# Kernel tuning notes

Measured on AMD Instinct MI355X. Metric: run time of the kernel, lower is better.

Reference implementation:

```python
import jax, jax.numpy as jnp
import numpy as np

N_NODES = 100000
N_EDGES = 1600000
D_IN = 128
D_HID = 128
D_OUT = 40


def _linear_init(key, fan_in, fan_out):
    # torch nn.Linear default: U(-1/sqrt(fan_in), 1/sqrt(fan_in)) for W and b
    kw, kb = jax.random.split(key)
    bound = 1.0 / np.sqrt(fan_in)
    W = jax.random.uniform(kw, (fan_in, fan_out), jnp.float32, -bound, bound)
    b = jax.random.uniform(kb, (fan_out,), jnp.float32, -bound, bound)
    return W, b


def setup_inputs() -> dict:
    key = jax.random.key(0)
    ks = jax.random.split(key, 8)
    x = jax.random.normal(ks[0], (N_NODES, D_IN), jnp.float32)
    edges = jax.random.randint(ks[1], (2, N_EDGES), 0, N_NODES, jnp.int64)
    # layer 0: MLP(128 -> 128 -> 128)
    W1_0, b1_0 = _linear_init(ks[2], D_IN, D_HID)
    W2_0, b2_0 = _linear_init(ks[3], D_HID, D_HID)
    # layer 1: MLP(128 -> 128 -> 128)
    W1_1, b1_1 = _linear_init(ks[4], D_HID, D_HID)
    W2_1, b2_1 = _linear_init(ks[5], D_HID, D_HID)
    # layer 2: MLP(128 -> 128 -> 40)
    W1_2, b1_2 = _linear_init(ks[6], D_HID, D_HID)
    W2_2, b2_2 = _linear_init(ks[7], D_HID, D_OUT)
    eps = jnp.zeros(())  # GINConv train_eps=True initializes eps=0
    return {
        "x": x, "edges": edges,
        "W1_0": W1_0, "b1_0": b1_0, "W2_0": W2_0, "b2_0": b2_0, "eps_0": eps,
        "W1_1": W1_1, "b1_1": b1_1, "W2_1": W2_1, "b2_1": b2_1, "eps_1": eps,
        "W1_2": W1_2, "b1_2": b1_2, "W2_2": W2_2, "b2_2": b2_2, "eps_2": eps,
    }


def _gin_conv(x, src, dst, eps, W1, b1, W2, b2):
    # sum-aggregate neighbor features: out_i = MLP((1+eps)*x_i + sum_{j->i} x_j)
    aggr = jax.ops.segment_sum(x[src], dst, num_segments=x.shape[0])
    h = (1.0 + eps) * x + aggr
    h = jnp.maximum(h @ W1 + b1, 0.0)  # MLP layer 1 + ReLU
    return h @ W2 + b2                  # MLP layer 2


def reference(x, edges,
              W1_0, b1_0, W2_0, b2_0, eps_0,
              W1_1, b1_1, W2_1, b2_1, eps_1,
              W1_2, b1_2, W2_2, b2_2, eps_2):
    src, dst = edges[0], edges[1]
    # dropout is identity at inference (training=False)
    h = jax.nn.relu(_gin_conv(x, src, dst, eps_0, W1_0, b1_0, W2_0, b2_0))
    h = jax.nn.relu(_gin_conv(h, src, dst, eps_1, W1_1, b1_1, W2_1, b2_1))
    o = _gin_conv(h, src, dst, eps_2, W1_2, b1_2, W2_2, b2_2)
    return jax.nn.log_softmax(o, axis=1)
```

## Files before the change

kernel.cpp:

```cpp
#include <hip/hip_runtime.h>
#include <stdint.h>

typedef __attribute__((ext_vector_type(8))) short short8;
typedef __attribute__((ext_vector_type(4))) short short4v;
typedef __attribute__((ext_vector_type(4))) float float4v;

__device__ __forceinline__ float bf2f(unsigned short s) {
    union { unsigned int u; float f; } c; c.u = ((unsigned int)s) << 16; return c.f;
}
__device__ __forceinline__ unsigned short f2bf(float f) {
    union { float f; unsigned int u; } c; c.f = f;
    unsigned int x = c.u;
    unsigned int r = x + 0x7fffu + ((x >> 16) & 1u);
    return (unsigned short)(r >> 16);
}
__device__ __forceinline__ void unpack2(unsigned int u, float& lo, float& hi) {
    union { unsigned int uu; float ff; } a, b;
    a.uu = u << 16;
    b.uu = u & 0xffff0000u;
    lo = a.ff; hi = b.ff;
}


__global__ __launch_bounds__(512) void bs_scan(const int* __restrict__ bucketCnt,
                                               int* __restrict__ bucketBase,
                                               int* __restrict__ bucketCur,
                                               int* __restrict__ off, int M, int nE) {
    __shared__ int s[512];
    int t = threadIdx.x;
    int v = bucketCnt[t];
    s[t] = v;
    __syncthreads();
    for (int o = 1; o < 512; o <<= 1) {
        int x = (t >= o) ? s[t - o] : 0;
        __syncthreads();
        s[t] += x;
        __syncthreads();
    }
    bucketBase[t] = s[t] - v;
    bucketCur[t] = s[t] - v;
    if (t == 511) bucketBase[512] = s[511];
    if (t == 0) off[M] = nE;
}

__global__ __launch_bounds__(512) void bs_scatter(const int* __restrict__ src,
                                                  const int* __restrict__ dst, int nE,
                                                  int* __restrict__ bucketCur,
                                                  unsigned int* __restrict__ ebuf) {
    __shared__ int cnt[512];
    __shared__ int excl[512];
    __shared__ int chunk[512];
    __shared__ unsigned int buf[4096];
    __shared__ unsigned short bkt[4096];
    int t = threadIdx.x;
    cnt[t] = 0;
    __syncthreads();
    int base = blockIdx.x * 4096;
    int n = nE - base; if (n > 4096) n = 4096;
    unsigned int pk[8]; int bk[8]; int rk[8];
#pragma unroll
    for (int u = 0; u < 8; ++u) {
        int i = t + u * 512;
        if (i < n) {
            int e = base + i;
            int d = dst[e];
            int b = d >> 8;
            bk[u] = b;
            pk[u] = (unsigned int)src[e] | ((unsigned int)(d & 255) << 17);
            rk[u] = atomicAdd(&cnt[b], 1);
        } else bk[u] = -1;
    }
    __syncthreads();
    excl[t] = cnt[t];
    __syncthreads();
    for (int o = 1; o < 512; o <<= 1) {
        int x = (t >= o) ? excl[t - o] : 0;
        __syncthreads();
        excl[t] += x;
        __syncthreads();
    }
    int ex = excl[t] - cnt[t];
    __syncthreads();
    excl[t] = ex;
    if (cnt[t]) chunk[t] = atomicAdd(&bucketCur[t], cnt[t]);
    __syncthreads();
#pragma unroll
    for (int u = 0; u < 8; ++u) {
        if (bk[u] >= 0) {
            int lp = excl[bk[u]] + rk[u];
            buf[lp] = pk[u];
            bkt[lp] = (unsigned short)bk[u];
        }
    }
    __syncthreads();
    for (int i = t; i < n; i += 512) {
        int b = bkt[i];
        ebuf[chunk[b] + (i - excl[b])] = buf[i];
    }
}

__global__ __launch_bounds__(512) void bs_build(const unsigned int* __restrict__ ebuf,
                                                const int* __restrict__ bucketBase,
                                                int* __restrict__ off,
                                                int* __restrict__ esrc, int M) {
    __shared__ int cnt[256];
    __shared__ int excl[256];
    __shared__ int obuf[5120];
    int t = threadIdx.x, b = blockIdx.x;
    int base = bucketBase[b];
    int n = bucketBase[b + 1] - base;
    if (t < 256) cnt[t] = 0;
    __syncthreads();
    unsigned int pk[10]; int dl[10]; int rk[10];
#pragma unroll
    for (int u = 0; u < 10; ++u) {
        int i = t + u * 512;
        if (i < n) {
            unsigned int p = ebuf[base + i];
            pk[u] = p;
            int d = (p >> 17) & 255;
            dl[u] = d;
            rk[u] = atomicAdd(&cnt[d], 1);
        } else dl[u] = -1;
    }
    __syncthreads();
    if (t < 256) excl[t] = cnt[t];
    __syncthreads();
    for (int o = 1; o < 256; o <<= 1) {
        int x = (t < 256 && t >= o) ? excl[t - o] : 0;
        __syncthreads();
        if (t < 256) excl[t] += x;
        __syncthreads();
    }
    if (t < 256) {
        int ex = excl[t] - cnt[t];
        int node = b * 256 + t;
        if (node < M) off[node] = base + ex;
        excl[t] = ex;
    }
    __syncthreads();
#pragma unroll
    for (int u = 0; u < 10; ++u) {
        if (dl[u] >= 0) {
            int lp = excl[dl[u]] + rk[u];
            if (lp < 5120) obuf[lp] = (int)(pk[u] & 0x1FFFF);
        }
    }
    __syncthreads();
    for (int i = t; i < n; i += 512) esrc[base + i] = obuf[i];
}

struct Prep {
    const float* W[6];
    unsigned short* hi[6];
    const float4* xin;
    uint2* xout;
    int n4;
    int nxBlocks;
    const int* dst;
    int nE;
    int* bucketCnt;
};

__global__ __launch_bounds__(256) void k_prep(Prep p) {
    __shared__ int c[512];
    int b = blockIdx.x;
    int t = threadIdx.x;
    if (b < 344) {
        int mat = b >> 6;
        int rel = b - mat * 64;
        int NPAD = (mat == 5) ? 48 : 128;
        int N = (mat == 5) ? 40 : 128;
        int idx = rel * 256 + t;
        if (idx >= NPAD * 128) return;
        int n = idx >> 7, k = idx & 127;
        float w = (n < N) ? p.W[mat][k * N + n] : 0.f;
        p.hi[mat][idx] = f2bf(w);
    } else if (b < 344 + p.nxBlocks) {
        int i = (b - 344) * 256 + t;
        if (i >= p.n4) return;
        float4 v = p.xin[i];
        uint2 o;
        o.x = ((unsigned int)f2bf(v.y) << 16) | f2bf(v.x);
        o.y = ((unsigned int)f2bf(v.w) << 16) | f2bf(v.z);
        p.xout[i] = o;
    } else {
        for (int i = t; i < 512; i += 256) c[i] = 0;
        __syncthreads();
        int base = (b - 344 - p.nxBlocks) * 4096;
        for (int i = t; i < 4096; i += 256) {
            int e = base + i;
            if (e < p.nE) atomicAdd(&c[p.dst[e] >> 8], 1);
        }
        __syncthreads();
        for (int i = t; i < 512; i += 256)
            if (c[i]) atomicAdd(&p.bucketCnt[i], c[i]);
    }
}

__device__ __forceinline__ void acc8(uint4 v, float* s) {
    float a, b;
    unpack2(v.x, a, b); s[0] += a; s[1] += b;
    unpack2(v.y, a, b); s[2] += a; s[3] += b;
    unpack2(v.z, a, b); s[4] += a; s[5] += b;
    unpack2(v.w, a, b); s[6] += a; s[7] += b;
}

__global__ __launch_bounds__(256) void k_aggr(const uint4* __restrict__ Hin,
                                              const int* __restrict__ off,
                                              const int* __restrict__ esrc,
                                              const float* __restrict__ epsp,
                                              uint4* __restrict__ Ahi, int M) {
    int w = threadIdx.x >> 6, lane = threadIdx.x & 63;
    int li = lane & 15, q = lane >> 4;
    int node = blockIdx.x * 16 + w * 4 + q;
    if (node >= M) return;
    float ep = 1.0f + epsp[0];
    uint4 ow = Hin[node * 16 + li];
    float s[8] = {0.f, 0.f, 0.f, 0.f, 0.f, 0.f, 0.f, 0.f};
    int i = off[node], e = off[node + 1];
    int idx[8];
    if (i + 8 <= e) {
#pragma unroll
        for (int j = 0; j < 8; ++j) idx[j] = esrc[i + j];
    }
    while (i + 8 <= e) {
        uint4 v[8];
#pragma unroll
        for (int j = 0; j < 8; ++j) v[j] = Hin[idx[j] * 16 + li];
        int inext = i + 8;
        if (inext + 8 <= e) {
#pragma unroll
            for (int j = 0; j < 8; ++j) idx[j] = esrc[inext + j];
        }
#pragma unroll
        for (int j = 0; j < 8; ++j) acc8(v[j], s);
        i = inext;
    }
    if (i < e) {
        int last = e - 1;
        uint4 v[8];
#pragma unroll
        for (int j = 0; j < 8; ++j) {
            int k = i + j;
            int cl = k < last ? k : last;
            v[j] = Hin[esrc[cl] * 16 + li];
        }
#pragma unroll
        for (int j = 0; j < 8; ++j) {
            bool ok = (i + j) < e;
            uint4 u;
            u.x = ok ? v[j].x : 0u;
            u.y = ok ? v[j].y : 0u;
            u.z = ok ? v[j].z : 0u;
            u.w = ok ? v[j].w : 0u;
            acc8(u, s);
        }
    }
    float o[8];
    unpack2(ow.x, o[0], o[1]);
    unpack2(ow.y, o[2], o[3]);
    unpack2(ow.z, o[4], o[5]);
    unpack2(ow.w, o[6], o[7]);
#pragma unroll
    for (int k = 0; k < 8; ++k) s[k] = ep * o[k] + s[k];
    uint4 r;
    r.x = ((unsigned int)f2bf(s[1]) << 16) | f2bf(s[0]);
    r.y = ((unsigned int)f2bf(s[3]) << 16) | f2bf(s[2]);
    r.z = ((unsigned int)f2bf(s[5]) << 16) | f2bf(s[4]);
    r.w = ((unsigned int)f2bf(s[7]) << 16) | f2bf(s[6]);
    Ahi[node * 16 + li] = r;
}

template <int NT2, bool LOGITS>
__global__ __launch_bounds__(256, 3) void k_mlp(const unsigned short* __restrict__ AhiS,
                                                const unsigned short* __restrict__ W1h,
                                                const float* __restrict__ B1,
                                                const unsigned short* __restrict__ W2h,
                                                const float* __restrict__ B2,
                                                unsigned short* __restrict__ HOut,
                                                float* __restrict__ LOut, int M) {
    __shared__ short wbuf[128 * 136];
    int t = threadIdx.x, w = t >> 6, lane = t & 63;
    int lm = lane & 15, lg = lane >> 4;
    int rbase = blockIdx.x * 128;

    short8 xf2[2][4];
    bool act[2];
#pragma unroll
    for (int t2 = 0; t2 < 2; ++t2) {
        int r0 = rbase + t2 * 64 + w * 16;
        act[t2] = (r0 < M);
        if (act[t2]) {
            const short* Xp = (const short*)AhiS + (r0 + lm) * 128 + lg * 8;
#pragma unroll
            for (int kb = 0; kb < 4; ++kb) xf2[t2][kb] = *(const short8*)(Xp + kb * 32);
        } else {
#pragma unroll
            for (int kb = 0; kb < 4; ++kb) xf2[t2][kb] = (short8){0,0,0,0,0,0,0,0};
        }
    }
    constexpr int W2CH = (NT2 * 16 * 128) / 2048;
    short8 w1r[8], w2r[W2CH];
#pragma unroll
    for (int u = 0; u < 8; ++u) w1r[u] = *(const short8*)(W1h + t * 8 + u * 2048);
#pragma unroll
    for (int u = 0; u < W2CH; ++u) w2r[u] = *(const short8*)(W2h + t * 8 + u * 2048);

#pragma unroll
    for (int u = 0; u < 8; ++u) {
        int i = t * 8 + u * 2048;
        *(short8*)&wbuf[(i >> 7) * 136 + (i & 127)] = w1r[u];
    }
    __syncthreads();

    short4v h2[2][8];
#pragma unroll
    for (int t2 = 0; t2 < 2; ++t2) {
        float4v acc1[8];
#pragma unroll
        for (int nt = 0; nt < 8; ++nt) acc1[nt] = (float4v){0.f, 0.f, 0.f, 0.f};
#pragma unroll
        for (int nt = 0; nt < 8; ++nt) {
#pragma unroll
            for (int kb = 0; kb < 4; ++kb) {
                short8 wf = *(const short8*)&wbuf[(nt * 16 + lm) * 136 + kb * 32 + lg * 8];
                acc1[nt] = __builtin_amdgcn_mfma_f32_16x16x32_bf16(wf, xf2[t2][kb], acc1[nt], 0, 0, 0);
            }
        }
#pragma unroll
        for (int nt = 0; nt < 8; ++nt) {
            float4 b1 = *(const float4*)(B1 + nt * 16 + lg * 4);
            float v0 = acc1[nt][0] + b1.x; v0 = v0 > 0.f ? v0 : 0.f;
            float v1 = acc1[nt][1] + b1.y; v1 = v1 > 0.f ? v1 : 0.f;
            float v2 = acc1[nt][2] + b1.z; v2 = v2 > 0.f ? v2 : 0.f;
            float v3 = acc1[nt][3] + b1.w; v3 = v3 > 0.f ? v3 : 0.f;
            h2[t2][nt] = (short4v){(short)f2bf(v0), (short)f2bf(v1),
                                   (short)f2bf(v2), (short)f2bf(v3)};
        }
    }

    __syncthreads();
#pragma unroll
    for (int u = 0; u < W2CH; ++u) {
        int i = t * 8 + u * 2048;
        *(short8*)&wbuf[(i >> 7) * 136 + (i & 127)] = w2r[u];
    }
    __syncthreads();

    float4v acc2[2][NT2];
#pragma unroll
    for (int t2 = 0; t2 < 2; ++t2)
#pragma unroll
        for (int ot = 0; ot < NT2; ++ot) acc2[t2][ot] = (float4v){0.f, 0.f, 0.f, 0.f};
#pragma unroll
    for (int ot = 0; ot < NT2; ++ot) {
#pragma unroll
        for (int nt = 0; nt < 8; ++nt) {
            short4v wf = *(const short4v*)&wbuf[(ot * 16 + lm) * 136 + nt * 16 + lg * 4];
#pragma unroll
            for (int t2 = 0; t2 < 2; ++t2)
                acc2[t2][ot] = __builtin_amdgcn_mfma_f32_16x16x16bf16_1k(wf, h2[t2][nt],
                                                                         acc2[t2][ot], 0, 0, 0);
        }
    }

#pragma unroll
    for (int t2 = 0; t2 < 2; ++t2) {
        if (!act[t2]) continue;
        int row = rbase + t2 * 64 + w * 16 + lm;
        if (!LOGITS) {
#pragma unroll
            for (int ot = 0; ot < NT2; ++ot) {
                float4 b2 = *(const float4*)(B2 + ot * 16 + lg * 4);
                float v0 = acc2[t2][ot][0] + b2.x; v0 = v0 > 0.f ? v0 : 0.f;
                float v1 = acc2[t2][ot][1] + b2.y; v1 = v1 > 0.f ? v1 : 0.f;
                float v2 = acc2[t2][ot][2] + b2.z; v2 = v2 > 0.f ? v2 : 0.f;
                float v3 = acc2[t2][ot][3] + b2.w; v3 = v3 > 0.f ? v3 : 0.f;
                uint2 pk;
                pk.x = ((unsigned int)f2bf(v1) << 16) | f2bf(v0);
                pk.y = ((unsigned int)f2bf(v3) << 16) | f2bf(v2);
                *(uint2*)(HOut + row * 128 + ot * 16 + lg * 4) = pk;
            }
        } else {
            float vv[NT2][4];
#pragma unroll
            for (int ot = 0; ot < NT2; ++ot) {
                int ub = ot * 16 + lg * 4;
                bool valid = ub <= 36;
                float4 b2 = valid ? *(const float4*)(B2 + ub) : (float4){0.f, 0.f, 0.f, 0.f};
                vv[ot][0] = valid ? acc2[t2][ot][0] + b2.x : -1e30f;
                vv[ot][1] = valid ? acc2[t2][ot][1] + b2.y : -1e30f;
                vv[ot][2] = valid ? acc2[t2][ot][2] + b2.z : -1e30f;
                vv[ot][3] = valid ? acc2[t2][ot][3] + b2.w : -1e30f;
            }
            float m = -1e30f;
#pragma unroll
            for (int ot = 0; ot < NT2; ++ot)
#pragma unroll
                for (int r = 0; r < 4; ++r) m = fmaxf(m, vv[ot][r]);
            m = fmaxf(m, __shfl_xor(m, 16, 64));
            m = fmaxf(m, __shfl_xor(m, 32, 64));
            float s = 0.f;
#pragma unroll
            for (int ot = 0; ot < NT2; ++ot)
#pragma unroll
                for (int r = 0; r < 4; ++r)
                    s += (vv[ot][r] > -1e29f) ? expf(vv[ot][r] - m) : 0.f;
            s += __shfl_xor(s, 16, 64);
            s += __shfl_xor(s, 32, 64);
            float ls = m + logf(s);
#pragma unroll
            for (int ot = 0; ot < NT2; ++ot) {
                int ub = ot * 16 + lg * 4;
                if (ub <= 36) {
                    float4 outv = {vv[ot][0] - ls, vv[ot][1] - ls,
                                   vv[ot][2] - ls, vv[ot][3] - ls};
                    *(float4*)(LOut + row * 40 + ub) = outv;
                }
            }
        }
    }
}

extern "C" void kernel_launch(void* const* d_in, const int* in_sizes, int n_in,
                              void* d_out, int out_size, void* d_ws, size_t ws_size,
                              hipStream_t stream) {
    const float* x    = (const float*)d_in[0];
    const int*   edges = (const int*)d_in[1];
    const float* eps0 = (const float*)d_in[6];
    const float* eps1 = (const float*)d_in[11];
    const float* eps2 = (const float*)d_in[16];
    const float* B1[3] = {(const float*)d_in[3], (const float*)d_in[8], (const float*)d_in[13]};
    const float* B2[3] = {(const float*)d_in[5], (const float*)d_in[10], (const float*)d_in[15]};

    int M  = in_sizes[0] / 128;
    int nE = in_sizes[1] / 2;
    const int* e_src = edges;
    const int* e_dst = edges + nE;

    char* ws = (char*)d_ws;
    size_t o = 0;
    auto alloc = [&](size_t bytes) {
        size_t p = o;
        o = (o + bytes + 511) & ~(size_t)511;
        return ws + p;
    };
    int* bucketCnt  = (int*)alloc(512 * 4);
    int* bucketBase = (int*)alloc(513 * 4);
    int* bucketCur  = (int*)alloc(512 * 4);
    int* off  = (int*)alloc((size_t)(M + 1) * 4);
    int* esrc = (int*)alloc((size_t)nE * 4);
    unsigned int* ebuf = (unsigned int*)alloc((size_t)nE * 4);

    Prep pp;
    pp.W[0] = (const float*)d_in[2];  pp.W[1] = (const float*)d_in[4];
    pp.W[2] = (const float*)d_in[7];  pp.W[3] = (const float*)d_in[9];
    pp.W[4] = (const float*)d_in[12]; pp.W[5] = (const float*)d_in[14];
    for (int m = 0; m < 6; ++m) {
        int npad = (m == 5) ? 48 : 128;
        pp.hi[m] = (unsigned short*)alloc((size_t)npad * 128 * 2);
    }
    unsigned short* xb  = (unsigned short*)alloc((size_t)M * 128 * 2);
    unsigned short* Ahi = (unsigned short*)alloc((size_t)M * 128 * 2);
    unsigned short* Hb  = (unsigned short*)alloc((size_t)M * 128 * 2);
    pp.xin = (const float4*)x;
    pp.xout = (uint2*)xb;
    pp.n4 = M * 32;
    pp.nxBlocks = (pp.n4 + 255) / 256;
    pp.dst = e_dst;
    pp.nE = nE;
    pp.bucketCnt = bucketCnt;
    (void)ws_size; (void)n_in; (void)out_size;

    int nChunk = (nE + 4095) / 4096;
    int nBk = (M + 255) / 256;

    hipMemsetAsync(bucketCnt, 0, 512 * 4, stream);
    k_prep<<<344 + pp.nxBlocks + nChunk, 256, 0, stream>>>(pp);
    bs_scan<<<1, 512, 0, stream>>>(bucketCnt, bucketBase, bucketCur, off, M, nE);
    bs_scatter<<<nChunk, 512, 0, stream>>>(e_src, e_dst, nE, bucketCur, ebuf);
    bs_build<<<nBk, 512, 0, stream>>>(ebuf, bucketBase, off, esrc, M);

    int gA = (M + 15) / 16;
    int gG = (M + 127) / 128;

    k_aggr<<<gA, 256, 0, stream>>>((const uint4*)xb, off, esrc, eps0, (uint4*)Ahi, M);
    k_mlp<8, false><<<gG, 256, 0, stream>>>(Ahi, pp.hi[0], B1[0],
                                            pp.hi[1], B2[0], Hb, nullptr, M);
    k_aggr<<<gA, 256, 0, stream>>>((const uint4*)Hb, off, esrc, eps1, (uint4*)Ahi, M);
    k_mlp<8, false><<<gG, 256, 0, stream>>>(Ahi, pp.hi[2], B1[1],
                                            pp.hi[3], B2[1], Hb, nullptr, M);
    k_aggr<<<gA, 256, 0, stream>>>((const uint4*)Hb, off, esrc, eps2, (uint4*)Ahi, M);
    k_mlp<3, true><<<gG, 256, 0, stream>>>(Ahi, pp.hi[4], B1[2],
                                           pp.hi[5], B2[2], nullptr,
                                           (float*)d_out, M);
}
```

Baseline: 411.2 us.

## Double-buffer neighbor gathers in aggregation and widen MLP blocks to 512 threads

The aggregation kernel now keeps two register batches of eight neighbor rows in flight, so the next gather overlaps the accumulation of the current one. The MLP kernel moves to 512-thread blocks that cover 256 rows each and share one staged weight tile. This amortises the weight loads into LDS over twice as many rows. The doubled gather buffers raise register pressure in k_aggr, which may lower occupancy. The larger MLP blocks also have fewer blocks to schedule.

```diff
diff --git a/kernel.cpp b/kernel.cpp
--- a/kernel.cpp
+++ b/kernel.cpp
@@ -5,9 +5,6 @@
 typedef __attribute__((ext_vector_type(4))) short short4v;
 typedef __attribute__((ext_vector_type(4))) float float4v;
 
-__device__ __forceinline__ float bf2f(unsigned short s) {
-    union { unsigned int u; float f; } c; c.u = ((unsigned int)s) << 16; return c.f;
-}
 __device__ __forceinline__ unsigned short f2bf(float f) {
     union { float f; unsigned int u; } c; c.f = f;
     unsigned int x = c.u;
@@ -20,134 +17,264 @@
     b.uu = u & 0xffff0000u;
     lo = a.ff; hi = b.ff;
 }
-
-
-__global__ __launch_bounds__(512) void bs_scan(const int* __restrict__ bucketCnt,
-                                               int* __restrict__ bucketBase,
-                                               int* __restrict__ bucketCur,
-                                               int* __restrict__ off, int M, int nE) {
-    __shared__ int s[512];
-    int t = threadIdx.x;
-    int v = bucketCnt[t];
-    s[t] = v;
-    __syncthreads();
-    for (int o = 1; o < 512; o <<= 1) {
-        int x = (t >= o) ? s[t - o] : 0;
-        __syncthreads();
-        s[t] += x;
-        __syncthreads();
-    }
-    bucketBase[t] = s[t] - v;
-    bucketCur[t] = s[t] - v;
-    if (t == 511) bucketBase[512] = s[511];
-    if (t == 0) off[M] = nE;
-}
-
-__global__ __launch_bounds__(512) void bs_scatter(const int* __restrict__ src,
-                                                  const int* __restrict__ dst, int nE,
-                                                  int* __restrict__ bucketCur,
-                                                  unsigned int* __restrict__ ebuf) {
-    __shared__ int cnt[512];
-    __shared__ int excl[512];
-    __shared__ int chunk[512];
-    __shared__ unsigned int buf[4096];
-    __shared__ unsigned short bkt[4096];
-    int t = threadIdx.x;
-    cnt[t] = 0;
-    __syncthreads();
-    int base = blockIdx.x * 4096;
-    int n = nE - base; if (n > 4096) n = 4096;
-    unsigned int pk[8]; int bk[8]; int rk[8];
-#pragma unroll
-    for (int u = 0; u < 8; ++u) {
-        int i = t + u * 512;
-        if (i < n) {
-            int e = base + i;
-            int d = dst[e];
-            int b = d >> 8;
-            bk[u] = b;
-            pk[u] = (unsigned int)src[e] | ((unsigned int)(d & 255) << 17);
-            rk[u] = atomicAdd(&cnt[b], 1);
-        } else bk[u] = -1;
-    }
-    __syncthreads();
-    excl[t] = cnt[t];
-    __syncthreads();
-    for (int o = 1; o < 512; o <<= 1) {
-        int x = (t >= o) ? excl[t - o] : 0;
-        __syncthreads();
-        excl[t] += x;
-        __syncthreads();
-    }
-    int ex = excl[t] - cnt[t];
-    __syncthreads();
-    excl[t] = ex;
-    if (cnt[t]) chunk[t] = atomicAdd(&bucketCur[t], cnt[t]);
-    __syncthreads();
-#pragma unroll
-    for (int u = 0; u < 8; ++u) {
-        if (bk[u] >= 0) {
-            int lp = excl[bk[u]] + rk[u];
-            buf[lp] = pk[u];
-            bkt[lp] = (unsigned short)bk[u];
-        }
-    }
-    __syncthreads();
-    for (int i = t; i < n; i += 512) {
-        int b = bkt[i];
-        ebuf[chunk[b] + (i - excl[b])] = buf[i];
-    }
-}
-
-__global__ __launch_bounds__(512) void bs_build(const unsigned int* __restrict__ ebuf,
-                                                const int* __restrict__ bucketBase,
-                                                int* __restrict__ off,
-                                                int* __restrict__ esrc, int M) {
-    __shared__ int cnt[256];
-    __shared__ int excl[256];
-    __shared__ int obuf[5120];
-    int t = threadIdx.x, b = blockIdx.x;
-    int base = bucketBase[b];
-    int n = bucketBase[b + 1] - base;
-    if (t < 256) cnt[t] = 0;
-    __syncthreads();
-    unsigned int pk[10]; int dl[10]; int rk[10];
-#pragma unroll
-    for (int u = 0; u < 10; ++u) {
-        int i = t + u * 512;
-        if (i < n) {
-            unsigned int p = ebuf[base + i];
-            pk[u] = p;
-            int d = (p >> 17) & 255;
-            dl[u] = d;
-            rk[u] = atomicAdd(&cnt[d], 1);
-        } else dl[u] = -1;
-    }
-    __syncthreads();
-    if (t < 256) excl[t] = cnt[t];
-    __syncthreads();
-    for (int o = 1; o < 256; o <<= 1) {
-        int x = (t < 256 && t >= o) ? excl[t - o] : 0;
-        __syncthreads();
-        if (t < 256) excl[t] += x;
-        __syncthreads();
-    }
-    if (t < 256) {
-        int ex = excl[t] - cnt[t];
-        int node = b * 256 + t;
-        if (node < M) off[node] = base + ex;
-        excl[t] = ex;
-    }
-    __syncthreads();
-#pragma unroll
-    for (int u = 0; u < 10; ++u) {
-        if (dl[u] >= 0) {
-            int lp = excl[dl[u]] + rk[u];
-            if (lp < 5120) obuf[lp] = (int)(pk[u] & 0x1FFFF);
-        }
-    }
-    __syncthreads();
-    for (int i = t; i < n; i += 512) esrc[base + i] = obuf[i];
+__device__ __forceinline__ void acc8(uint4 v, float* s) {
+    float a, b;
+    unpack2(v.x, a, b); s[0] += a; s[1] += b;
+    unpack2(v.y, a, b); s[2] += a; s[3] += b;
+    unpack2(v.z, a, b); s[4] += a; s[5] += b;
+    unpack2(v.w, a, b); s[6] += a; s[7] += b;
+}
+
+__global__ __launch_bounds__(256) void k_aggr(const uint4* __restrict__ Hin,
+                                              const int* __restrict__ off,
+                                              const int* __restrict__ esrc,
+                                              const float* __restrict__ epsp,
+                                              uint4* __restrict__ Ahi, int M) {
+    int w = threadIdx.x >> 6, lane = threadIdx.x & 63;
+    int li = lane & 15, q = lane >> 4;
+    int node = blockIdx.x * 16 + w * 4 + q;
+    if (node >= M) return;
+    float ep = 1.0f + epsp[0];
+    uint4 ow = Hin[node * 16 + li];
+    float s[8] = {0.f, 0.f, 0.f, 0.f, 0.f, 0.f, 0.f, 0.f};
+    int i0 = off[node], e = off[node + 1];
+    int nb = (e - i0) >> 3;
+    uint4 va[8], vb[8];
+    int idc[8], idn[8];
+
+    if (nb > 0) {
+#pragma unroll
+        for (int j = 0; j < 8; ++j) idc[j] = esrc[i0 + j];
+#pragma unroll
+        for (int j = 0; j < 8; ++j) va[j] = Hin[idc[j] * 16 + li];
+        if (nb > 1) {
+#pragma unroll
+            for (int j = 0; j < 8; ++j) idn[j] = esrc[i0 + 8 + j];
+        }
+        int b = 1;
+        while (b + 1 < nb) {
+#pragma unroll
+            for (int j = 0; j < 8; ++j) vb[j] = Hin[idn[j] * 16 + li];
+#pragma unroll
+            for (int j = 0; j < 8; ++j) idc[j] = esrc[i0 + (b + 1) * 8 + j];
+#pragma unroll
+            for (int j = 0; j < 8; ++j) acc8(va[j], s);
+#pragma unroll
+            for (int j = 0; j < 8; ++j) va[j] = Hin[idc[j] * 16 + li];
+            if (b + 2 < nb) {
+#pragma unroll
+                for (int j = 0; j < 8; ++j) idn[j] = esrc[i0 + (b + 2) * 8 + j];
+            }
+#pragma unroll
+            for (int j = 0; j < 8; ++j) acc8(vb[j], s);
+            b += 2;
+        }
+        if (b < nb) {
+#pragma unroll
+            for (int j = 0; j < 8; ++j) vb[j] = Hin[idn[j] * 16 + li];
+#pragma unroll
+            for (int j = 0; j < 8; ++j) acc8(va[j], s);
+#pragma unroll
+            for (int j = 0; j < 8; ++j) acc8(vb[j], s);
+        } else {
+#pragma unroll
+            for (int j = 0; j < 8; ++j) acc8(va[j], s);
+        }
+    }
+    int i = i0 + nb * 8;
+    if (i < e) {
+        int last = e - 1;
+        uint4 v[8];
+#pragma unroll
+        for (int j = 0; j < 8; ++j) {
+            int k = i + j;
+            int cl = k < last ? k : last;
+            v[j] = Hin[esrc[cl] * 16 + li];
+        }
+#pragma unroll
+        for (int j = 0; j < 8; ++j) {
+            bool ok = (i + j) < e;
+            uint4 u2;
+            u2.x = ok ? v[j].x : 0u;
+            u2.y = ok ? v[j].y : 0u;
+            u2.z = ok ? v[j].z : 0u;
+            u2.w = ok ? v[j].w : 0u;
+            acc8(u2, s);
+        }
+    }
+    float o[8];
+    unpack2(ow.x, o[0], o[1]);
+    unpack2(ow.y, o[2], o[3]);
+    unpack2(ow.z, o[4], o[5]);
+    unpack2(ow.w, o[6], o[7]);
+#pragma unroll
+    for (int k = 0; k < 8; ++k) s[k] = ep * o[k] + s[k];
+    uint4 r;
+    r.x = ((unsigned int)f2bf(s[1]) << 16) | f2bf(s[0]);
+    r.y = ((unsigned int)f2bf(s[3]) << 16) | f2bf(s[2]);
+    r.z = ((unsigned int)f2bf(s[5]) << 16) | f2bf(s[4]);
+    r.w = ((unsigned int)f2bf(s[7]) << 16) | f2bf(s[6]);
+    Ahi[node * 16 + li] = r;
+}
+
+template <int NT2, bool LOGITS>
+__global__ __launch_bounds__(512, 4) void k_mlp(const unsigned short* __restrict__ AhiS,
+                                                const unsigned short* __restrict__ W1h,
+                                                const float* __restrict__ B1,
+                                                const unsigned short* __restrict__ W2h,
+                                                const float* __restrict__ B2,
+                                                unsigned short* __restrict__ HOut,
+                                                float* __restrict__ LOut, int M) {
+    __shared__ short wbuf[128 * 136];
+    int t = threadIdx.x, w = t >> 6, lane = t & 63;
+    int lm = lane & 15, lg = lane >> 4;
+    int h = w >> 2, wq = w & 3;
+    int nTP = (M + 255) / 256;
+    for (int tp = blockIdx.x; tp < nTP; tp += gridDim.x) {
+        __syncthreads();
+        int rbase = tp * 256 + h * 128;
+
+        short8 xf2[2][4];
+        bool act[2];
+#pragma unroll
+        for (int t2 = 0; t2 < 2; ++t2) {
+            int r0 = rbase + t2 * 64 + wq * 16;
+            act[t2] = (r0 < M);
+            if (act[t2]) {
+                const short* Xp = (const short*)AhiS + (r0 + lm) * 128 + lg * 8;
+#pragma unroll
+                for (int kb = 0; kb < 4; ++kb) xf2[t2][kb] = *(const short8*)(Xp + kb * 32);
+            } else {
+#pragma unroll
+                for (int kb = 0; kb < 4; ++kb) xf2[t2][kb] = (short8){0,0,0,0,0,0,0,0};
+            }
+        }
+        constexpr int WTOT2 = NT2 * 16 * 128;
+        constexpr int W2CH = (WTOT2 + 4095) / 4096;
+        short8 w1r[4], w2r[W2CH];
+#pragma unroll
+        for (int u = 0; u < 4; ++u) w1r[u] = *(const short8*)(W1h + t * 8 + u * 4096);
+#pragma unroll
+        for (int u = 0; u < W2CH; ++u) {
+            int i = t * 8 + u * 4096;
+            if (i < WTOT2) w2r[u] = *(const short8*)(W2h + i);
+        }
+
+#pragma unroll
+        for (int u = 0; u < 4; ++u) {
+            int i = t * 8 + u * 4096;
+            *(short8*)&wbuf[(i >> 7) * 136 + (i & 127)] = w1r[u];
+        }
+        __syncthreads();
+
+        short4v h2[2][8];
+#pragma unroll
+        for (int t2 = 0; t2 < 2; ++t2) {
+            float4v acc1[8];
+#pragma unroll
+            for (int nt = 0; nt < 8; ++nt) acc1[nt] = (float4v){0.f, 0.f, 0.f, 0.f};
+#pragma unroll
+            for (int nt = 0; nt < 8; ++nt) {
+#pragma unroll
+                for (int kb = 0; kb < 4; ++kb) {
+                    short8 wf = *(const short8*)&wbuf[(nt * 16 + lm) * 136 + kb * 32 + lg * 8];
+                    acc1[nt] = __builtin_amdgcn_mfma_f32_16x16x32_bf16(wf, xf2[t2][kb], acc1[nt], 0, 0, 0);
+                }
+            }
+#pragma unroll
+            for (int nt = 0; nt < 8; ++nt) {
+                float4 b1 = *(const float4*)(B1 + nt * 16 + lg * 4);
+                float v0 = acc1[nt][0] + b1.x; v0 = v0 > 0.f ? v0 : 0.f;
+                float v1 = acc1[nt][1] + b1.y; v1 = v1 > 0.f ? v1 : 0.f;
+                float v2 = acc1[nt][2] + b1.z; v2 = v2 > 0.f ? v2 : 0.f;
+                float v3 = acc1[nt][3] + b1.w; v3 = v3 > 0.f ? v3 : 0.f;
+                h2[t2][nt] = (short4v){(short)f2bf(v0), (short)f2bf(v1),
+                                       (short)f2bf(v2), (short)f2bf(v3)};
+            }
+        }
+
+        __syncthreads();
+#pragma unroll
+        for (int u = 0; u < W2CH; ++u) {
+            int i = t * 8 + u * 4096;
+            if (i < WTOT2) *(short8*)&wbuf[(i >> 7) * 136 + (i & 127)] = w2r[u];
+        }
+        __syncthreads();
+
+        float4v acc2[2][NT2];
+#pragma unroll
+        for (int t2 = 0; t2 < 2; ++t2)
+#pragma unroll
+            for (int ot = 0; ot < NT2; ++ot) acc2[t2][ot] = (float4v){0.f, 0.f, 0.f, 0.f};
+#pragma unroll
+        for (int ot = 0; ot < NT2; ++ot) {
+#pragma unroll
+            for (int nt = 0; nt < 8; ++nt) {
+                short4v wf = *(const short4v*)&wbuf[(ot * 16 + lm) * 136 + nt * 16 + lg * 4];
+#pragma unroll
+                for (int t2 = 0; t2 < 2; ++t2)
+                    acc2[t2][ot] = __builtin_amdgcn_mfma_f32_16x16x16bf16_1k(wf, h2[t2][nt],
+                                                                             acc2[t2][ot], 0, 0, 0);
+            }
+        }
+
+#pragma unroll
+        for (int t2 = 0; t2 < 2; ++t2) {
+            if (!act[t2]) continue;
+            int row = rbase + t2 * 64 + wq * 16 + lm;
+            if (!LOGITS) {
+#pragma unroll
+                for (int ot = 0; ot < NT2; ++ot) {
+                    float4 b2 = *(const float4*)(B2 + ot * 16 + lg * 4);
+                    float v0 = acc2[t2][ot][0] + b2.x; v0 = v0 > 0.f ? v0 : 0.f;
+                    float v1 = acc2[t2][ot][1] + b2.y; v1 = v1 > 0.f ? v1 : 0.f;
+                    float v2 = acc2[t2][ot][2] + b2.z; v2 = v2 > 0.f ? v2 : 0.f;
+                    float v3 = acc2[t2][ot][3] + b2.w; v3 = v3 > 0.f ? v3 : 0.f;
+                    uint2 pk;
+                    pk.x = ((unsigned int)f2bf(v1) << 16) | f2bf(v0);
+                    pk.y = ((unsigned int)f2bf(v3) << 16) | f2bf(v2);
+                    *(uint2*)(HOut + row * 128 + ot * 16 + lg * 4) = pk;
+                }
+            } else {
+                float vv[NT2][4];
+#pragma unroll
+                for (int ot = 0; ot < NT2; ++ot) {
+                    int ub = ot * 16 + lg * 4;
+                    bool valid = ub <= 36;
+                    float4 b2 = valid ? *(const float4*)(B2 + ub) : (float4){0.f, 0.f, 0.f, 0.f};
+                    vv[ot][0] = valid ? acc2[t2][ot][0] + b2.x : -1e30f;
+                    vv[ot][1] = valid ? acc2[t2][ot][1] + b2.y : -1e30f;
+                    vv[ot][2] = valid ? acc2[t2][ot][2] + b2.z : -1e30f;
+                    vv[ot][3] = valid ? acc2[t2][ot][3] + b2.w : -1e30f;
+                }
+                float m = -1e30f;
+#pragma unroll
+                for (int ot = 0; ot < NT2; ++ot)
+#pragma unroll
+                    for (int r = 0; r < 4; ++r) m = fmaxf(m, vv[ot][r]);
+                m = fmaxf(m, __shfl_xor(m, 16, 64));
+                m = fmaxf(m, __shfl_xor(m, 32, 64));
+                float s = 0.f;
+#pragma unroll
+                for (int ot = 0; ot < NT2; ++ot)
+#pragma unroll
+                    for (int r = 0; r < 4; ++r)
+                        s += (vv[ot][r] > -1e29f) ? expf(vv[ot][r] - m) : 0.f;
+                s += __shfl_xor(s, 16, 64);
+                s += __shfl_xor(s, 32, 64);
+                float ls = m + logf(s);
+#pragma unroll
+                for (int ot = 0; ot < NT2; ++ot) {
+                    int ub = ot * 16 + lg * 4;
+                    if (ub <= 36) {
+                        float4 outv = {vv[ot][0] - ls, vv[ot][1] - ls,
+                                       vv[ot][2] - ls, vv[ot][3] - ls};
+                        *(float4*)(LOut + row * 40 + ub) = outv;
+                    }
+                }
+            }
+        }
+    }
 }
 
 struct Prep {
@@ -198,229 +325,132 @@
     }
 }
 
-__device__ __forceinline__ void acc8(uint4 v, float* s) {
-    float a, b;
-    unpack2(v.x, a, b); s[0] += a; s[1] += b;
-    unpack2(v.y, a, b); s[2] += a; s[3] += b;
-    unpack2(v.z, a, b); s[4] += a; s[5] += b;
-    unpack2(v.w, a, b); s[6] += a; s[7] += b;
-}
-
-__global__ __launch_bounds__(256) void k_aggr(const uint4* __restrict__ Hin,
-                                              const int* __restrict__ off,
-                                              const int* __restrict__ esrc,
-                                              const float* __restrict__ epsp,
-                                              uint4* __restrict__ Ahi, int M) {
-    int w = threadIdx.x >> 6, lane = threadIdx.x & 63;
-    int li = lane & 15, q = lane >> 4;
-    int node = blockIdx.x * 16 + w * 4 + q;
-    if (node >= M) return;
-    float ep = 1.0f + epsp[0];
-    uint4 ow = Hin[node * 16 + li];
-    float s[8] = {0.f, 0.f, 0.f, 0.f, 0.f, 0.f, 0.f, 0.f};
-    int i = off[node], e = off[node + 1];
-    int idx[8];
-    if (i + 8 <= e) {
-#pragma unroll
-        for (int j = 0; j < 8; ++j) idx[j] = esrc[i + j];
-    }
-    while (i + 8 <= e) {
-        uint4 v[8];
-#pragma unroll
-        for (int j = 0; j < 8; ++j) v[j] = Hin[idx[j] * 16 + li];
-        int inext = i + 8;
-        if (inext + 8 <= e) {
-#pragma unroll
-            for (int j = 0; j < 8; ++j) idx[j] = esrc[inext + j];
-        }
-#pragma unroll
-        for (int j = 0; j < 8; ++j) acc8(v[j], s);
-        i = inext;
-    }
-    if (i < e) {
-        int last = e - 1;
-        uint4 v[8];
-#pragma unroll
-        for (int j = 0; j < 8; ++j) {
-            int k = i + j;
-            int cl = k < last ? k : last;
-            v[j] = Hin[esrc[cl] * 16 + li];
-        }
-#pragma unroll
-        for (int j = 0; j < 8; ++j) {
-            bool ok = (i + j) < e;
-            uint4 u;
-            u.x = ok ? v[j].x : 0u;
-            u.y = ok ? v[j].y : 0u;
-            u.z = ok ? v[j].z : 0u;
-            u.w = ok ? v[j].w : 0u;
-            acc8(u, s);
-        }
-    }
-    float o[8];
-    unpack2(ow.x, o[0], o[1]);
-    unpack2(ow.y, o[2], o[3]);
-    unpack2(ow.z, o[4], o[5]);
-    unpack2(ow.w, o[6], o[7]);
-#pragma unroll
-    for (int k = 0; k < 8; ++k) s[k] = ep * o[k] + s[k];
-    uint4 r;
-    r.x = ((unsigned int)f2bf(s[1]) << 16) | f2bf(s[0]);
-    r.y = ((unsigned int)f2bf(s[3]) << 16) | f2bf(s[2]);
-    r.z = ((unsigned int)f2bf(s[5]) << 16) | f2bf(s[4]);
-    r.w = ((unsigned int)f2bf(s[7]) << 16) | f2bf(s[6]);
-    Ahi[node * 16 + li] = r;
-}
-
-template <int NT2, bool LOGITS>
-__global__ __launch_bounds__(256, 3) void k_mlp(const unsigned short* __restrict__ AhiS,
-                                                const unsigned short* __restrict__ W1h,
-                                                const float* __restrict__ B1,
-                                                const unsigned short* __restrict__ W2h,
-                                                const float* __restrict__ B2,
-                                                unsigned short* __restrict__ HOut,
-                                                float* __restrict__ LOut, int M) {
-    __shared__ short wbuf[128 * 136];
-    int t = threadIdx.x, w = t >> 6, lane = t & 63;
-    int lm = lane & 15, lg = lane >> 4;
-    int rbase = blockIdx.x * 128;
-
-    short8 xf2[2][4];
-    bool act[2];
-#pragma unroll
-    for (int t2 = 0; t2 < 2; ++t2) {
-        int r0 = rbase + t2 * 64 + w * 16;
-        act[t2] = (r0 < M);
-        if (act[t2]) {
-            const short* Xp = (const short*)AhiS + (r0 + lm) * 128 + lg * 8;
-#pragma unroll
-            for (int kb = 0; kb < 4; ++kb) xf2[t2][kb] = *(const short8*)(Xp + kb * 32);
-        } else {
-#pragma unroll
-            for (int kb = 0; kb < 4; ++kb) xf2[t2][kb] = (short8){0,0,0,0,0,0,0,0};
-        }
-    }
-    constexpr int W2CH = (NT2 * 16 * 128) / 2048;
-    short8 w1r[8], w2r[W2CH];
-#pragma unroll
-    for (int u = 0; u < 8; ++u) w1r[u] = *(const short8*)(W1h + t * 8 + u * 2048);
-#pragma unroll
-    for (int u = 0; u < W2CH; ++u) w2r[u] = *(const short8*)(W2h + t * 8 + u * 2048);
-
+__global__ __launch_bounds__(512) void bs_scan(const int* __restrict__ bucketCnt,
+                                               int* __restrict__ bucketBase,
+                                               int* __restrict__ bucketCur,
+                                               int* __restrict__ off, int M, int nE) {
+    __shared__ int s[512];
+    int t = threadIdx.x;
+    int v = bucketCnt[t];
+    s[t] = v;
+    __syncthreads();
+    for (int o = 1; o < 512; o <<= 1) {
+        int x = (t >= o) ? s[t - o] : 0;
+        __syncthreads();
+        s[t] += x;
+        __syncthreads();
+    }
+    bucketBase[t] = s[t] - v;
+    bucketCur[t] = s[t] - v;
+    if (t == 511) bucketBase[512] = s[511];
+    if (t == 0) off[M] = nE;
+}
+
+__global__ __launch_bounds__(512) void bs_scatter(const int* __restrict__ src,
+                                                  const int* __restrict__ dst, int nE,
+                                                  int* __restrict__ bucketCur,
+                                                  unsigned int* __restrict__ ebuf) {
+    __shared__ int cnt[512];
+    __shared__ int excl[512];
+    __shared__ int chunk[512];
+    __shared__ unsigned int buf[4096];
+    __shared__ unsigned short bkt[4096];
+    int t = threadIdx.x;
+    cnt[t] = 0;
+    __syncthreads();
+    int base = blockIdx.x * 4096;
+    int n = nE - base; if (n > 4096) n = 4096;
+    unsigned int pk[8]; int bk[8]; int rk[8];
 #pragma unroll
     for (int u = 0; u < 8; ++u) {
-        int i = t * 8 + u * 2048;
-        *(short8*)&wbuf[(i >> 7) * 136 + (i & 127)] = w1r[u];
-    }
-    __syncthreads();
-
-    short4v h2[2][8];
-#pragma unroll
-    for (int t2 = 0; t2 < 2; ++t2) {
-        float4v acc1[8];
-#pragma unroll
-        for (int nt = 0; nt < 8; ++nt) acc1[nt] = (float4v){0.f, 0.f, 0.f, 0.f};
-#pragma unroll
-        for (int nt = 0; nt < 8; ++nt) {
-#pragma unroll
-            for (int kb = 0; kb < 4; ++kb) {
-                short8 wf = *(const short8*)&wbuf[(nt * 16 + lm) * 136 + kb * 32 + lg * 8];
-                acc1[nt] = __builtin_amdgcn_mfma_f32_16x16x32_bf16(wf, xf2[t2][kb], acc1[nt], 0, 0, 0);
-            }
-        }
-#pragma unroll
-        for (int nt = 0; nt < 8; ++nt) {
-            float4 b1 = *(const float4*)(B1 + nt * 16 + lg * 4);
-            float v0 = acc1[nt][0] + b1.x; v0 = v0 > 0.f ? v0 : 0.f;
-            float v1 = acc1[nt][1] + b1.y; v1 = v1 > 0.f ? v1 : 0.f;
-            float v2 = acc1[nt][2] + b1.z; v2 = v2 > 0.f ? v2 : 0.f;
-            float v3 = acc1[nt][3] + b1.w; v3 = v3 > 0.f ? v3 : 0.f;
-            h2[t2][nt] = (short4v){(short)f2bf(v0), (short)f2bf(v1),
-                                   (short)f2bf(v2), (short)f2bf(v3)};
-        }
-    }
-
-    __syncthreads();
-#pragma unroll
-    for (int u = 0; u < W2CH; ++u) {
-        int i = t * 8 + u * 2048;
-        *(short8*)&wbuf[(i >> 7) * 136 + (i & 127)] = w2r[u];
-    }
-    __syncthreads();
-
-    float4v acc2[2][NT2];
-#pragma unroll
-    for (int t2 = 0; t2 < 2; ++t2)
-#pragma unroll
-        for (int ot = 0; ot < NT2; ++ot) acc2[t2][ot] = (float4v){0.f, 0.f, 0.f, 0.f};
-#pragma unroll
-    for (int ot = 0; ot < NT2; ++ot) {
-#pragma unroll
-        for (int nt = 0; nt < 8; ++nt) {
-            short4v wf = *(const short4v*)&wbuf[(ot * 16 + lm) * 136 + nt * 16 + lg * 4];
-#pragma unroll
-            for (int t2 = 0; t2 < 2; ++t2)
-                acc2[t2][ot] = __builtin_amdgcn_mfma_f32_16x16x16bf16_1k(wf, h2[t2][nt],
-                                                                         acc2[t2][ot], 0, 0, 0);
-        }
-    }
-
-#pragma unroll
-    for (int t2 = 0; t2 < 2; ++t2) {
-        if (!act[t2]) continue;
-        int row = rbase + t2 * 64 + w * 16 + lm;
-        if (!LOGITS) {
-#pragma unroll
-            for (int ot = 0; ot < NT2; ++ot) {
-                float4 b2 = *(const float4*)(B2 + ot * 16 + lg * 4);
-                float v0 = acc2[t2][ot][0] + b2.x; v0 = v0 > 0.f ? v0 : 0.f;
-                float v1 = acc2[t2][ot][1] + b2.y; v1 = v1 > 0.f ? v1 : 0.f;
-                float v2 = acc2[t2][ot][2] + b2.z; v2 = v2 > 0.f ? v2 : 0.f;
-                float v3 = acc2[t2][ot][3] + b2.w; v3 = v3 > 0.f ? v3 : 0.f;
-                uint2 pk;
-                pk.x = ((unsigned int)f2bf(v1) << 16) | f2bf(v0);
-                pk.y = ((unsigned int)f2bf(v3) << 16) | f2bf(v2);
-                *(uint2*)(HOut + row * 128 + ot * 16 + lg * 4) = pk;
-            }
-        } else {
-            float vv[NT2][4];
-#pragma unroll
-            for (int ot = 0; ot < NT2; ++ot) {
-                int ub = ot * 16 + lg * 4;
-                bool valid = ub <= 36;
-                float4 b2 = valid ? *(const float4*)(B2 + ub) : (float4){0.f, 0.f, 0.f, 0.f};
-                vv[ot][0] = valid ? acc2[t2][ot][0] + b2.x : -1e30f;
-                vv[ot][1] = valid ? acc2[t2][ot][1] + b2.y : -1e30f;
-                vv[ot][2] = valid ? acc2[t2][ot][2] + b2.z : -1e30f;
-                vv[ot][3] = valid ? acc2[t2][ot][3] + b2.w : -1e30f;
-            }
-            float m = -1e30f;
-#pragma unroll
-            for (int ot = 0; ot < NT2; ++ot)
-#pragma unroll
-                for (int r = 0; r < 4; ++r) m = fmaxf(m, vv[ot][r]);
-            m = fmaxf(m, __shfl_xor(m, 16, 64));
-            m = fmaxf(m, __shfl_xor(m, 32, 64));
-            float s = 0.f;
-#pragma unroll
-            for (int ot = 0; ot < NT2; ++ot)
-#pragma unroll
-                for (int r = 0; r < 4; ++r)
-                    s += (vv[ot][r] > -1e29f) ? expf(vv[ot][r] - m) : 0.f;
-            s += __shfl_xor(s, 16, 64);
-            s += __shfl_xor(s, 32, 64);
-            float ls = m + logf(s);
-#pragma unroll
-            for (int ot = 0; ot < NT2; ++ot) {
-                int ub = ot * 16 + lg * 4;
-                if (ub <= 36) {
-                    float4 outv = {vv[ot][0] - ls, vv[ot][1] - ls,
-                                   vv[ot][2] - ls, vv[ot][3] - ls};
-                    *(float4*)(LOut + row * 40 + ub) = outv;
-                }
-            }
-        }
-    }
+        int i = t + u * 512;
+        if (i < n) {
+            int e = base + i;
+            int d = dst[e];
+            int b = d >> 8;
+            bk[u] = b;
+            pk[u] = (unsigned int)src[e] | ((unsigned int)(d & 255) << 17);
+            rk[u] = atomicAdd(&cnt[b], 1);
+        } else bk[u] = -1;
+    }
+    __syncthreads();
+    excl[t] = cnt[t];
+    __syncthreads();
+    for (int o = 1; o < 512; o <<= 1) {
+        int x = (t >= o) ? excl[t - o] : 0;
+        __syncthreads();
+        excl[t] += x;
+        __syncthreads();
+    }
+    int ex = excl[t] - cnt[t];
+    __syncthreads();
+    excl[t] = ex;
+    if (cnt[t]) chunk[t] = atomicAdd(&bucketCur[t], cnt[t]);
+    __syncthreads();
+#pragma unroll
+    for (int u = 0; u < 8; ++u) {
+        if (bk[u] >= 0) {
+            int lp = excl[bk[u]] + rk[u];
+            buf[lp] = pk[u];
+            bkt[lp] = (unsigned short)bk[u];
+        }
+    }
+    __syncthreads();
+    for (int i = t; i < n; i += 512) {
+        int b = bkt[i];
+        ebuf[chunk[b] + (i - excl[b])] = buf[i];
+    }
+}
+
+__global__ __launch_bounds__(512) void bs_build(const unsigned int* __restrict__ ebuf,
+                                                const int* __restrict__ bucketBase,
+                                                int* __restrict__ off,
+                                                int* __restrict__ esrc, int M) {
+    __shared__ int cnt[256];
+    __shared__ int excl[256];
+    __shared__ int obuf[5120];
+    int t = threadIdx.x, b = blockIdx.x;
+    int base = bucketBase[b];
+    int n = bucketBase[b + 1] - base;
+    if (t < 256) cnt[t] = 0;
+    __syncthreads();
+    unsigned int pk[10]; int dl[10]; int rk[10];
+#pragma unroll
+    for (int u = 0; u < 10; ++u) {
+        int i = t + u * 512;
+        if (i < n) {
+            unsigned int p = ebuf[base + i];
+            pk[u] = p;
+            int d = (p >> 17) & 255;
+            dl[u] = d;
+            rk[u] = atomicAdd(&cnt[d], 1);
+        } else dl[u] = -1;
+    }
+    __syncthreads();
+    if (t < 256) excl[t] = cnt[t];
+    __syncthreads();
+    for (int o = 1; o < 256; o <<= 1) {
+        int x = (t < 256 && t >= o) ? excl[t - o] : 0;
+        __syncthreads();
+        if (t < 256) excl[t] += x;
+        __syncthreads();
+    }
+    if (t < 256) {
+        int ex = excl[t] - cnt[t];
+        int node = b * 256 + t;
+        if (node < M) off[node] = base + ex;
+        excl[t] = ex;
+    }
+    __syncthreads();
+#pragma unroll
+    for (int u = 0; u < 10; ++u) {
+        if (dl[u] >= 0) {
+            int lp = excl[dl[u]] + rk[u];
+            if (lp < 5120) obuf[lp] = (int)(pk[u] & 0x1FFFF);
+        }
+    }
+    __syncthreads();
+    for (int i = t; i < n; i += 512) esrc[base + i] = obuf[i];
 }
 
 extern "C" void kernel_launch(void* const* d_in, const int* in_sizes, int n_in,
@@ -483,16 +513,16 @@
     bs_build<<<nBk, 512, 0, stream>>>(ebuf, bucketBase, off, esrc, M);
 
     int gA = (M + 15) / 16;
-    int gG = (M + 127) / 128;
+    int nTP = (M + 255) / 256;
 
     k_aggr<<<gA, 256, 0, stream>>>((const uint4*)xb, off, esrc, eps0, (uint4*)Ahi, M);
-    k_mlp<8, false><<<gG, 256, 0, stream>>>(Ahi, pp.hi[0], B1[0],
-                                            pp.hi[1], B2[0], Hb, nullptr, M);
+    k_mlp<8, false><<<nTP, 512, 0, stream>>>(Ahi, pp.hi[0], B1[0],
+                                             pp.hi[1], B2[0], Hb, nullptr, M);
     k_aggr<<<gA, 256, 0, stream>>>((const uint4*)Hb, off, esrc, eps1, (uint4*)Ahi, M);
-    k_mlp<8, false><<<gG, 256, 0, stream>>>(Ahi, pp.hi[2], B1[1],
-                                            pp.hi[3], B2[1], Hb, nullptr, M);
+    k_mlp<8, false><<<nTP, 512, 0, stream>>>(Ahi, pp.hi[2], B1[1],
+                                             pp.hi[3], B2[1], Hb, nullptr, M);
     k_aggr<<<gA, 256, 0, stream>>>((const uint4*)Hb, off, esrc, eps2, (uint4*)Ahi, M);
-    k_mlp<3, true><<<gG, 256, 0, stream>>>(Ahi, pp.hi[4], B1[2],
-                                           pp.hi[5], B2[2], nullptr,
-                                           (float*)d_out, M);
-}
+    k_mlp<3, true><<<nTP, 512, 0, stream>>>(Ahi, pp.hi[4], B1[2],
+                                            pp.hi[5], B2[2], nullptr,
+                                            (float*)d_out, M);
+}
```

Result: slower. 511.5 us (+24.4%).
